# Kernel optimization log

Hardware: AMD Instinct MI355X
Metric: run time of the kernel (lower is better)

## Reference

```python
import jax, jax.numpy as jnp
import numpy as np

N_NODES = 100000
N_EDGES = 1600000
D = 128
BN_EPS = 1e-5

def setup_inputs() -> dict:
    key = jax.random.key(0)
    ks = jax.random.split(key, 6)
    h = jax.random.normal(ks[0], (N_NODES, D), dtype=jnp.float32)
    src = jax.random.randint(ks[1], (N_EDGES,), 0, N_NODES, dtype=jnp.int32)
    dst = jax.random.randint(ks[2], (N_EDGES,), 0, N_NODES, dtype=jnp.int32)
    eps = jnp.zeros((1,), dtype=jnp.float32)
    # 2-layer GIN apply_func MLP, scaled for stable activations
    W1 = jax.random.normal(ks[3], (D, D), dtype=jnp.float32) / np.sqrt(D)
    b1 = jnp.zeros((D,), dtype=jnp.float32)
    W2 = jax.random.normal(ks[4], (D, D), dtype=jnp.float32) / np.sqrt(D)
    b2 = jnp.zeros((D,), dtype=jnp.float32)
    gamma = jnp.ones((D,), dtype=jnp.float32)
    beta = jnp.zeros((D,), dtype=jnp.float32)
    return {"h": h, "src": src, "dst": dst, "eps": eps,
            "W1": W1, "b1": b1, "W2": W2, "b2": b2,
            "gamma": gamma, "beta": beta}

def reference(h, src, dst, eps, W1, b1, W2, b2, gamma, beta):
    # --- neighbor sum aggregation: update_all(copy_u('h'), fn.sum) ---
    msgs = h[src]                                   # [E, D] irregular gather
    neigh = jax.ops.segment_sum(msgs, dst, num_segments=N_NODES)  # [N, D]
    # --- eps-scaled self term ---
    x = (1.0 + eps[0]) * h + neigh                  # [N, D]
    # --- apply_func: 2-layer MLP ---
    x = jax.nn.relu(x @ W1 + b1)
    x = x @ W2 + b2
    # --- BatchNorm1d over node dim (training-mode batch stats) ---
    mean = jnp.mean(x, axis=0)
    var = jnp.mean(jnp.square(x - mean), axis=0)
    x = (x - mean) * jax.lax.rsqrt(var + BN_EPS) * gamma + beta
    # --- activation + residual ---
    x = jax.nn.relu(x)
    x = h + x  # residual (in_dim == out_dim)
    return x
```

## Files before the change

kernel.cpp:

```cpp
#include <hip/hip_runtime.h>

#define NN 100000
#define NE 1600000
#define DD 128
#define BN_EPS 1e-5f

#define SBSH 9
#define SBSZ 512
#define NSB ((NN + SBSZ - 1) / SBSZ)
#define CAPS 9216
#define SCATBLKS 512
#define EPB ((NE + SCATBLKS - 1) / SCATBLKS)
#define PREPBLKS 512
#define GRID_PS (SCATBLKS + PREPBLKS)
#define BN_BLOCKS 1024

typedef __attribute__((ext_vector_type(8))) short short8;
typedef __attribute__((ext_vector_type(4))) float floatx4;

__device__ __forceinline__ unsigned short f2bf(float f) {
    union { float f; unsigned u; } v; v.f = f;
    return (unsigned short)((v.u + 0x7FFFu + ((v.u >> 16) & 1u)) >> 16);
}
__device__ __forceinline__ float bf2f(unsigned short u) {
    union { unsigned u; float f; } v; v.u = ((unsigned)u) << 16;
    return v.f;
}

__global__ __launch_bounds__(256) void prep_scatter_kernel(
    const float* __restrict__ W1, const float* __restrict__ W2,
    unsigned short* __restrict__ W1t, unsigned short* __restrict__ W2t,
    const float* __restrict__ h, unsigned short* __restrict__ hb, int do_hb,
    const int* __restrict__ src, const int* __restrict__ dst,
    int* __restrict__ scnt, int* __restrict__ sbuf)
{
    __shared__ int bins[256];
    int t = threadIdx.x;

    if (blockIdx.x < SCATBLKS) {
        bins[t] = 0;
        __syncthreads();
        int base = blockIdx.x * EPB;
        int ecnt = min(EPB, NE - base);
        for (int i = t; i < ecnt; i += 256)
            atomicAdd(&bins[dst[base + i] >> SBSH], 1);
        __syncthreads();
        int c = bins[t];
        int gb = (t < NSB && c) ? atomicAdd(&scnt[t], c) : 0;
        __syncthreads();
        bins[t] = t * CAPS + gb;
        __syncthreads();
        for (int i = t; i < ecnt; i += 256) {
            int d = dst[base + i];
            int p = atomicAdd(&bins[d >> SBSH], 1);
            sbuf[p] = (src[base + i] << SBSH) | (d & (SBSZ - 1));
        }
    } else {
        int tid0 = (blockIdx.x - SCATBLKS) * 256 + t;
        int stride = PREPBLKS * 256;
        for (int i = tid0; i < DD * DD; i += stride) {
            int n = i >> 7, k = i & 127;
            W1t[i] = f2bf(W1[k * DD + n]);
            W2t[i] = f2bf(W2[k * DD + n]);
        }
        if (do_hb) {
            const float4* h4 = (const float4*)h;
            ushort4* hb4 = (ushort4*)hb;
            for (int i = tid0; i < NN * (DD / 4); i += stride) {
                float4 v = h4[i];
                ushort4 o;
                o.x = f2bf(v.x); o.y = f2bf(v.y); o.z = f2bf(v.z); o.w = f2bf(v.w);
                hb4[i] = o;
            }
        }
    }
}

__global__ __launch_bounds__(1024) void permute_kernel(
    const int* __restrict__ scnt, int* __restrict__ sbuf,
    int2* __restrict__ off2)
{
    __shared__ int ew[CAPS];
    __shared__ int cnt[SBSZ];
    __shared__ int cur[SBSZ];
    __shared__ int stmp[SBSZ];
    int sb = blockIdx.x, t = threadIdx.x;
    if (t < SBSZ) cnt[t] = 0;
    __syncthreads();
    int n = min(scnt[sb], CAPS);
    int sbase = sb * CAPS;
    for (int i = t; i < n; i += 1024) {
        int e = sbuf[sbase + i];
        ew[i] = e;
        atomicAdd(&cnt[e & (SBSZ - 1)], 1);
    }
    __syncthreads();
    int c = 0;
    if (t < SBSZ) { c = cnt[t]; stmp[t] = c; }
    __syncthreads();
#pragma unroll
    for (int ofs = 1; ofs < SBSZ; ofs <<= 1) {
        int u = (t < SBSZ && t >= ofs) ? stmp[t - ofs] : 0;
        __syncthreads();
        if (t < SBSZ) stmp[t] += u;
        __syncthreads();
    }
    if (t < SBSZ) {
        int excl = stmp[t] - c;
        cur[t] = excl;
        off2[sb * SBSZ + t] = make_int2(sbase + excl, sbase + excl + c);
    }
    __syncthreads();
    for (int i = t; i < n; i += 1024) {
        int e = ew[i];
        int p = atomicAdd(&cur[e & (SBSZ - 1)], 1);
        sbuf[sbase + p] = e >> SBSH;
    }
}

__global__ __launch_bounds__(256) void gather_bf16_kernel(
    const float* __restrict__ h, const unsigned short* __restrict__ hb,
    const float* __restrict__ eps, const int2* __restrict__ off2,
    const int* __restrict__ srcs, unsigned short* __restrict__ xb)
{
    int node = blockIdx.x * 16 + (threadIdx.x >> 4);
    if (node >= NN) return;
    int c8 = threadIdx.x & 15;
    const float s = 1.0f + eps[0];
    const float4* h4 = (const float4*)h;
    float4 a0 = h4[node * 32 + c8 * 2];
    float4 a1 = h4[node * 32 + c8 * 2 + 1];
    float acc[8] = {s * a0.x, s * a0.y, s * a0.z, s * a0.w,
                    s * a1.x, s * a1.y, s * a1.z, s * a1.w};
    int2 oo = off2[node];
    int e = oo.x, eend = oo.y;
    const short8* hb8 = (const short8*)hb;
    for (; e + 3 < eend; e += 4) {
        int s0 = srcs[e],     s1 = srcs[e + 1];
        int s2 = srcs[e + 2], s3 = srcs[e + 3];
        short8 v0 = hb8[s0 * 16 + c8];
        short8 v1 = hb8[s1 * 16 + c8];
        short8 v2 = hb8[s2 * 16 + c8];
        short8 v3 = hb8[s3 * 16 + c8];
#pragma unroll
        for (int j = 0; j < 8; ++j) {
            float t0 = bf2f((unsigned short)v0[j]) + bf2f((unsigned short)v1[j]);
            float t1 = bf2f((unsigned short)v2[j]) + bf2f((unsigned short)v3[j]);
            acc[j] += t0 + t1;
        }
    }
    for (; e < eend; ++e) {
        short8 v0 = hb8[srcs[e] * 16 + c8];
#pragma unroll
        for (int j = 0; j < 8; ++j) acc[j] += bf2f((unsigned short)v0[j]);
    }
    short8 o;
#pragma unroll
    for (int j = 0; j < 8; ++j) o[j] = (short)f2bf(acc[j]);
    ((short8*)xb)[node * 16 + c8] = o;
}

__global__ __launch_bounds__(256) void gather_f32_kernel(
    const float* __restrict__ h, const float* __restrict__ eps,
    const int2* __restrict__ off2, const int* __restrict__ srcs,
    unsigned short* __restrict__ xb)
{
    int node = blockIdx.x * 16 + (threadIdx.x >> 4);
    if (node >= NN) return;
    int c8 = threadIdx.x & 15;
    const float4* h4 = (const float4*)h;
    const float s = 1.0f + eps[0];
    float4 a0 = h4[node * 32 + c8 * 2];
    float4 a1 = h4[node * 32 + c8 * 2 + 1];
    float acc[8] = {s * a0.x, s * a0.y, s * a0.z, s * a0.w,
                    s * a1.x, s * a1.y, s * a1.z, s * a1.w};
    int2 oo = off2[node];
    int e = oo.x, eend = oo.y;
    for (; e + 1 < eend; e += 2) {
        int s0 = srcs[e], s1 = srcs[e + 1];
        float4 u0 = h4[s0 * 32 + c8 * 2], u1 = h4[s0 * 32 + c8 * 2 + 1];
        float4 w0 = h4[s1 * 32 + c8 * 2], w1 = h4[s1 * 32 + c8 * 2 + 1];
        acc[0] += u0.x + w0.x; acc[1] += u0.y + w0.y;
        acc[2] += u0.z + w0.z; acc[3] += u0.w + w0.w;
        acc[4] += u1.x + w1.x; acc[5] += u1.y + w1.y;
        acc[6] += u1.z + w1.z; acc[7] += u1.w + w1.w;
    }
    if (e < eend) {
        int s0 = srcs[e];
        float4 u0 = h4[s0 * 32 + c8 * 2], u1 = h4[s0 * 32 + c8 * 2 + 1];
        acc[0] += u0.x; acc[1] += u0.y; acc[2] += u0.z; acc[3] += u0.w;
        acc[4] += u1.x; acc[5] += u1.y; acc[6] += u1.z; acc[7] += u1.w;
    }
    short8 o;
#pragma unroll
    for (int j = 0; j < 8; ++j) o[j] = (short)f2bf(acc[j]);
    ((short8*)xb)[node * 16 + c8] = o;
}

__global__ __launch_bounds__(512) void mlp_fused_kernel(
    const unsigned short* __restrict__ X,
    const unsigned short* __restrict__ W1t, const unsigned short* __restrict__ W2t,
    const float* __restrict__ b1, const float* __restrict__ b2,
    unsigned short* __restrict__ Y, float* __restrict__ stats)
{
    extern __shared__ char smem[];
    unsigned short* wl = (unsigned short*)smem;
    unsigned short* xl = (unsigned short*)(smem + 34816);

    const int tid = threadIdx.x;
    const int r0 = blockIdx.x * 128;
    const int lane = tid & 63;
    const int wv = tid >> 6;
    const int m = lane & 15;
    const int hi = lane >> 4;

    const short8* W18 = (const short8*)W1t;
#pragma unroll
    for (int l = 0; l < 4; ++l) {
        int idx = tid + l * 512;
        int n = idx >> 4, c = idx & 15;
        *(short8*)&wl[n * 136 + c * 8] = W18[idx];
    }
    const short8* X8 = (const short8*)X;
#pragma unroll
    for (int l = 0; l < 4; ++l) {
        int idx = tid + l * 512;
        int row = idx >> 4, c = idx & 15;
        int g = r0 + row;
        short8 v = {0, 0, 0, 0, 0, 0, 0, 0};
        if (g < NN) v = X8[g * 16 + c];
        *(short8*)&xl[row * 136 + c * 8] = v;
    }
    __syncthreads();

    floatx4 acc[8];
#pragma unroll
    for (int i = 0; i < 8; ++i) acc[i] = (floatx4){0.f, 0.f, 0.f, 0.f};
#pragma unroll
    for (int kc = 0; kc < 4; ++kc) {
        short8 a = *(const short8*)&xl[(wv * 16 + m) * 136 + kc * 32 + hi * 8];
#pragma unroll
        for (int nt = 0; nt < 8; ++nt) {
            short8 b = *(const short8*)&wl[(nt * 16 + m) * 136 + kc * 32 + hi * 8];
            acc[nt] = __builtin_amdgcn_mfma_f32_16x16x32_bf16(a, b, acc[nt], 0, 0, 0);
        }
    }
    __syncthreads();

#pragma unroll
    for (int nt = 0; nt < 8; ++nt) {
        float bv = b1[nt * 16 + m];
#pragma unroll
        for (int r = 0; r < 4; ++r) {
            float v = fmaxf(acc[nt][r] + bv, 0.f);
            xl[(wv * 16 + hi * 4 + r) * 136 + nt * 16 + m] = f2bf(v);
        }
    }
    const short8* W28 = (const short8*)W2t;
#pragma unroll
    for (int l = 0; l < 4; ++l) {
        int idx = tid + l * 512;
        int n = idx >> 4, c = idx & 15;
        *(short8*)&wl[n * 136 + c * 8] = W28[idx];
    }
    __syncthreads();

#pragma unroll
    for (int i = 0; i < 8; ++i) acc[i] = (floatx4){0.f, 0.f, 0.f, 0.f};
#pragma unroll
    for (int kc = 0; kc < 4; ++kc) {
        short8 a = *(const short8*)&xl[(wv * 16 + m) * 136 + kc * 32 + hi * 8];
#pragma unroll
        for (int nt = 0; nt < 8; ++nt) {
            short8 b = *(const short8*)&wl[(nt * 16 + m) * 136 + kc * 32 + hi * 8];
            acc[nt] = __builtin_amdgcn_mfma_f32_16x16x32_bf16(a, b, acc[nt], 0, 0, 0);
        }
    }
    __syncthreads();

#pragma unroll
    for (int nt = 0; nt < 8; ++nt) {
        float bv = b2[nt * 16 + m];
#pragma unroll
        for (int r = 0; r < 4; ++r) {
            float v = acc[nt][r] + bv;
            xl[(wv * 16 + hi * 4 + r) * 136 + nt * 16 + m] = f2bf(v);
        }
    }
    __syncthreads();

#pragma unroll
    for (int l = 0; l < 4; ++l) {
        int idx = tid + l * 512;
        int row = idx >> 4, c = idx & 15;
        int g = r0 + row;
        if (g < NN)
            ((short8*)Y)[g * 16 + c] = *(const short8*)&xl[row * 136 + c * 8];
    }

    int col = tid & 127, quarter = tid >> 7;
    int rlim = min(128, NN - r0);
    int rbeg = quarter * 32, rend = min(rbeg + 32, rlim);
    float s = 0.f, q = 0.f;
    for (int r = rbeg; r < rend; ++r) {
        float v = bf2f(xl[r * 136 + col]);
        s += v; q += v * v;
    }
    float* red = (float*)wl;
    red[tid] = s;
    red[512 + tid] = q;
    __syncthreads();
    if (tid < 128) {
        float ts = red[tid] + red[128 + tid] + red[256 + tid] + red[384 + tid];
        float tq = red[512 + tid] + red[640 + tid] + red[768 + tid] + red[896 + tid];
        atomicAdd(&stats[tid], ts);
        atomicAdd(&stats[DD + tid], tq);
    }
}

__global__ __launch_bounds__(256) void bn_final_kernel(
    const unsigned short* __restrict__ Y, const float* __restrict__ h,
    const float* __restrict__ gamma, const float* __restrict__ beta,
    const float* __restrict__ stats, float* __restrict__ out)
{
    const float invN = 1.0f / (float)NN;
    int t0 = blockIdx.x * 256 + threadIdx.x;
    int c8 = t0 & 15;
    float sc[8], sh[8];
#pragma unroll
    for (int j = 0; j < 8; ++j) {
        int col = c8 * 8 + j;
        float mu = stats[col] * invN;
        float var = stats[DD + col] * invN - mu * mu;
        float s = rsqrtf(var + BN_EPS) * gamma[col];
        sc[j] = s;
        sh[j] = beta[col] - mu * s;
    }
    const short8* Y8 = (const short8*)Y;
    const float4* H4 = (const float4*)h;
    float4* O4 = (float4*)out;
    const int total = NN * 16;
    const int stride = BN_BLOCKS * 256;
    for (int i = t0; i < total; i += stride) {
        short8 u = Y8[i];
        float4 h0 = H4[2 * i], h1 = H4[2 * i + 1];
        float4 r0, r1;
        r0.x = h0.x + fmaxf(bf2f((unsigned short)u[0]) * sc[0] + sh[0], 0.f);
        r0.y = h0.y + fmaxf(bf2f((unsigned short)u[1]) * sc[1] + sh[1], 0.f);
        r0.z = h0.z + fmaxf(bf2f((unsigned short)u[2]) * sc[2] + sh[2], 0.f);
        r0.w = h0.w + fmaxf(bf2f((unsigned short)u[3]) * sc[3] + sh[3], 0.f);
        r1.x = h1.x + fmaxf(bf2f((unsigned short)u[4]) * sc[4] + sh[4], 0.f);
        r1.y = h1.y + fmaxf(bf2f((unsigned short)u[5]) * sc[5] + sh[5], 0.f);
        r1.z = h1.z + fmaxf(bf2f((unsigned short)u[6]) * sc[6] + sh[6], 0.f);
        r1.w = h1.w + fmaxf(bf2f((unsigned short)u[7]) * sc[7] + sh[7], 0.f);
        O4[2 * i] = r0;
        O4[2 * i + 1] = r1;
    }
}

extern "C" void kernel_launch(void* const* d_in, const int* in_sizes, int n_in,
                              void* d_out, int out_size, void* d_ws, size_t ws_size,
                              hipStream_t stream)
{
    const float* h     = (const float*)d_in[0];
    const int*   src   = (const int*)d_in[1];
    const int*   dst   = (const int*)d_in[2];
    const float* eps   = (const float*)d_in[3];
    const float* W1    = (const float*)d_in[4];
    const float* b1    = (const float*)d_in[5];
    const float* W2    = (const float*)d_in[6];
    const float* b2    = (const float*)d_in[7];
    const float* gamma = (const float*)d_in[8];
    const float* beta  = (const float*)d_in[9];
    float* out = (float*)d_out;

    char* w = (char*)d_ws;
    size_t o = 0;
    float* stats    = (float*)(w + o); o += 256 * 4;
    int* scnt       = (int*)(w + o); o += 256 * 4;
    unsigned short* W1t = (unsigned short*)(w + o); o += (size_t)DD * DD * 2;
    unsigned short* W2t = (unsigned short*)(w + o); o += (size_t)DD * DD * 2;
    int2* off2      = (int2*)(w + o); o += (size_t)NSB * SBSZ * 8;
    int* sbuf       = (int*)(w + o); o += (size_t)NSB * CAPS * 4;
    unsigned short* xb  = (unsigned short*)(w + o); o += (size_t)NN * DD * 2;
    unsigned short* hb  = (unsigned short*)(w + o); o += (size_t)NN * DD * 2;
    const int use_hb = (ws_size >= o) ? 1 : 0;

    hipMemsetAsync(stats, 0, 512 * sizeof(int), stream);

    prep_scatter_kernel<<<GRID_PS, 256, 0, stream>>>(
        W1, W2, W1t, W2t, h, hb, use_hb, src, dst, scnt, sbuf);

    permute_kernel<<<NSB, 1024, 0, stream>>>(scnt, sbuf, off2);

    if (use_hb)
        gather_bf16_kernel<<<(NN + 15) / 16, 256, 0, stream>>>(h, hb, eps, off2, sbuf, xb);
    else
        gather_f32_kernel<<<(NN + 15) / 16, 256, 0, stream>>>(h, eps, off2, sbuf, xb);

    size_t gemm_lds = 69632;
    mlp_fused_kernel<<<(NN + 127) / 128, 512, gemm_lds, stream>>>(
        xb, W1t, W2t, b1, b2, xb, stats);

    bn_final_kernel<<<BN_BLOCKS, 256, 0, stream>>>(xb, h, gamma, beta, stats, out);
}
```

Baseline: 269.3 us.

## Fuse per-superblock edge permutation into gather kernel using LDS-resident edge lists

Removes the separate permute kernel and the off2 offset buffer. Each gather block now handles a quarter (128 nodes) of a 512-node superblock: it reads that superblock's bucket of edges twice, counts and scans the edges belonging to its quarter, places the source indices into shared memory, and then runs the node-wise gather from LDS. This saves one kernel launch and the global write and reread of the permuted edges, at the cost of each bucket being read four times and a 3072-entry LDS cap that could overflow if a quarter receives more edges.

```diff
diff --git a/kernel.cpp b/kernel.cpp
--- a/kernel.cpp
+++ b/kernel.cpp
@@ -13,6 +13,7 @@
 #define EPB ((NE + SCATBLKS - 1) / SCATBLKS)
 #define PREPBLKS 512
 #define GRID_PS (SCATBLKS + PREPBLKS)
+#define QCAP 3072
 #define BN_BLOCKS 1024
 
 typedef __attribute__((ext_vector_type(8))) short short8;
@@ -76,125 +77,118 @@
     }
 }
 
-__global__ __launch_bounds__(1024) void permute_kernel(
-    const int* __restrict__ scnt, int* __restrict__ sbuf,
-    int2* __restrict__ off2)
-{
-    __shared__ int ew[CAPS];
-    __shared__ int cnt[SBSZ];
-    __shared__ int cur[SBSZ];
-    __shared__ int stmp[SBSZ];
-    int sb = blockIdx.x, t = threadIdx.x;
-    if (t < SBSZ) cnt[t] = 0;
-    __syncthreads();
-    int n = min(scnt[sb], CAPS);
-    int sbase = sb * CAPS;
-    for (int i = t; i < n; i += 1024) {
+template <bool HB>
+__global__ __launch_bounds__(256) void permgather_kernel(
+    const float* __restrict__ h, const unsigned short* __restrict__ hb,
+    const float* __restrict__ eps, const int* __restrict__ scnt,
+    const int* __restrict__ sbuf, unsigned short* __restrict__ xb)
+{
+    __shared__ int es[QCAP];
+    __shared__ int cnt[128];
+    __shared__ int beg[128];
+    __shared__ int cur[128];
+
+    const int sub = blockIdx.x;
+    const int b = sub >> 2;
+    const int q = sub & 3;
+    const int t = threadIdx.x;
+
+    if (t < 128) cnt[t] = 0;
+    __syncthreads();
+
+    const int n = min(scnt[b], CAPS);
+    const int sbase = b * CAPS;
+
+    for (int i = t; i < n; i += 256) {
         int e = sbuf[sbase + i];
-        ew[i] = e;
-        atomicAdd(&cnt[e & (SBSZ - 1)], 1);
-    }
-    __syncthreads();
-    int c = 0;
-    if (t < SBSZ) { c = cnt[t]; stmp[t] = c; }
-    __syncthreads();
-#pragma unroll
-    for (int ofs = 1; ofs < SBSZ; ofs <<= 1) {
-        int u = (t < SBSZ && t >= ofs) ? stmp[t - ofs] : 0;
-        __syncthreads();
-        if (t < SBSZ) stmp[t] += u;
-        __syncthreads();
-    }
-    if (t < SBSZ) {
-        int excl = stmp[t] - c;
-        cur[t] = excl;
-        off2[sb * SBSZ + t] = make_int2(sbase + excl, sbase + excl + c);
-    }
-    __syncthreads();
-    for (int i = t; i < n; i += 1024) {
-        int e = ew[i];
-        int p = atomicAdd(&cur[e & (SBSZ - 1)], 1);
-        sbuf[sbase + p] = e >> SBSH;
-    }
-}
-
-__global__ __launch_bounds__(256) void gather_bf16_kernel(
-    const float* __restrict__ h, const unsigned short* __restrict__ hb,
-    const float* __restrict__ eps, const int2* __restrict__ off2,
-    const int* __restrict__ srcs, unsigned short* __restrict__ xb)
-{
-    int node = blockIdx.x * 16 + (threadIdx.x >> 4);
-    if (node >= NN) return;
-    int c8 = threadIdx.x & 15;
-    const float s = 1.0f + eps[0];
+        int nl = e & (SBSZ - 1);
+        if ((nl >> 7) == q) atomicAdd(&cnt[nl & 127], 1);
+    }
+    __syncthreads();
+
+    if (t < 128) beg[t] = cnt[t];
+    __syncthreads();
+#pragma unroll
+    for (int ofs = 1; ofs < 128; ofs <<= 1) {
+        int u = (t < 128 && t >= ofs) ? beg[t - ofs] : 0;
+        __syncthreads();
+        if (t < 128) beg[t] += u;
+        __syncthreads();
+    }
+    if (t < 128) {
+        int ex = beg[t] - cnt[t];
+        beg[t] = ex;
+        cur[t] = ex;
+    }
+    __syncthreads();
+
+    for (int i = t; i < n; i += 256) {
+        int e = sbuf[sbase + i];
+        int nl = e & (SBSZ - 1);
+        if ((nl >> 7) == q) {
+            int p = atomicAdd(&cur[nl & 127], 1);
+            es[p] = e >> SBSH;
+        }
+    }
+    __syncthreads();
+
+    const float sE = 1.0f + eps[0];
     const float4* h4 = (const float4*)h;
-    float4 a0 = h4[node * 32 + c8 * 2];
-    float4 a1 = h4[node * 32 + c8 * 2 + 1];
-    float acc[8] = {s * a0.x, s * a0.y, s * a0.z, s * a0.w,
-                    s * a1.x, s * a1.y, s * a1.z, s * a1.w};
-    int2 oo = off2[node];
-    int e = oo.x, eend = oo.y;
     const short8* hb8 = (const short8*)hb;
-    for (; e + 3 < eend; e += 4) {
-        int s0 = srcs[e],     s1 = srcs[e + 1];
-        int s2 = srcs[e + 2], s3 = srcs[e + 3];
-        short8 v0 = hb8[s0 * 16 + c8];
-        short8 v1 = hb8[s1 * 16 + c8];
-        short8 v2 = hb8[s2 * 16 + c8];
-        short8 v3 = hb8[s3 * 16 + c8];
-#pragma unroll
-        for (int j = 0; j < 8; ++j) {
-            float t0 = bf2f((unsigned short)v0[j]) + bf2f((unsigned short)v1[j]);
-            float t1 = bf2f((unsigned short)v2[j]) + bf2f((unsigned short)v3[j]);
-            acc[j] += t0 + t1;
-        }
-    }
-    for (; e < eend; ++e) {
-        short8 v0 = hb8[srcs[e] * 16 + c8];
-#pragma unroll
-        for (int j = 0; j < 8; ++j) acc[j] += bf2f((unsigned short)v0[j]);
-    }
-    short8 o;
-#pragma unroll
-    for (int j = 0; j < 8; ++j) o[j] = (short)f2bf(acc[j]);
-    ((short8*)xb)[node * 16 + c8] = o;
-}
-
-__global__ __launch_bounds__(256) void gather_f32_kernel(
-    const float* __restrict__ h, const float* __restrict__ eps,
-    const int2* __restrict__ off2, const int* __restrict__ srcs,
-    unsigned short* __restrict__ xb)
-{
-    int node = blockIdx.x * 16 + (threadIdx.x >> 4);
-    if (node >= NN) return;
-    int c8 = threadIdx.x & 15;
-    const float4* h4 = (const float4*)h;
-    const float s = 1.0f + eps[0];
-    float4 a0 = h4[node * 32 + c8 * 2];
-    float4 a1 = h4[node * 32 + c8 * 2 + 1];
-    float acc[8] = {s * a0.x, s * a0.y, s * a0.z, s * a0.w,
-                    s * a1.x, s * a1.y, s * a1.z, s * a1.w};
-    int2 oo = off2[node];
-    int e = oo.x, eend = oo.y;
-    for (; e + 1 < eend; e += 2) {
-        int s0 = srcs[e], s1 = srcs[e + 1];
-        float4 u0 = h4[s0 * 32 + c8 * 2], u1 = h4[s0 * 32 + c8 * 2 + 1];
-        float4 w0 = h4[s1 * 32 + c8 * 2], w1 = h4[s1 * 32 + c8 * 2 + 1];
-        acc[0] += u0.x + w0.x; acc[1] += u0.y + w0.y;
-        acc[2] += u0.z + w0.z; acc[3] += u0.w + w0.w;
-        acc[4] += u1.x + w1.x; acc[5] += u1.y + w1.y;
-        acc[6] += u1.z + w1.z; acc[7] += u1.w + w1.w;
-    }
-    if (e < eend) {
-        int s0 = srcs[e];
-        float4 u0 = h4[s0 * 32 + c8 * 2], u1 = h4[s0 * 32 + c8 * 2 + 1];
-        acc[0] += u0.x; acc[1] += u0.y; acc[2] += u0.z; acc[3] += u0.w;
-        acc[4] += u1.x; acc[5] += u1.y; acc[6] += u1.z; acc[7] += u1.w;
-    }
-    short8 o;
-#pragma unroll
-    for (int j = 0; j < 8; ++j) o[j] = (short)f2bf(acc[j]);
-    ((short8*)xb)[node * 16 + c8] = o;
+    const int c8 = t & 15;
+    const int node0 = b * SBSZ + (q << 7);
+#pragma unroll
+    for (int pass = 0; pass < 8; ++pass) {
+        int nl = pass * 16 + (t >> 4);
+        int node = node0 + nl;
+        if (node >= NN) continue;
+        float4 a0 = h4[node * 32 + c8 * 2];
+        float4 a1 = h4[node * 32 + c8 * 2 + 1];
+        float acc[8] = {sE * a0.x, sE * a0.y, sE * a0.z, sE * a0.w,
+                        sE * a1.x, sE * a1.y, sE * a1.z, sE * a1.w};
+        int e = beg[nl], eend = beg[nl] + cnt[nl];
+        if (HB) {
+            for (; e + 3 < eend; e += 4) {
+                int s0 = es[e],     s1 = es[e + 1];
+                int s2 = es[e + 2], s3 = es[e + 3];
+                short8 v0 = hb8[s0 * 16 + c8];
+                short8 v1 = hb8[s1 * 16 + c8];
+                short8 v2 = hb8[s2 * 16 + c8];
+                short8 v3 = hb8[s3 * 16 + c8];
+#pragma unroll
+                for (int j = 0; j < 8; ++j) {
+                    float t0 = bf2f((unsigned short)v0[j]) + bf2f((unsigned short)v1[j]);
+                    float t1 = bf2f((unsigned short)v2[j]) + bf2f((unsigned short)v3[j]);
+                    acc[j] += t0 + t1;
+                }
+            }
+            for (; e < eend; ++e) {
+                short8 v0 = hb8[es[e] * 16 + c8];
+#pragma unroll
+                for (int j = 0; j < 8; ++j) acc[j] += bf2f((unsigned short)v0[j]);
+            }
+        } else {
+            for (; e + 1 < eend; e += 2) {
+                int s0 = es[e], s1 = es[e + 1];
+                float4 u0 = h4[s0 * 32 + c8 * 2], u1 = h4[s0 * 32 + c8 * 2 + 1];
+                float4 w0 = h4[s1 * 32 + c8 * 2], w1 = h4[s1 * 32 + c8 * 2 + 1];
+                acc[0] += u0.x + w0.x; acc[1] += u0.y + w0.y;
+                acc[2] += u0.z + w0.z; acc[3] += u0.w + w0.w;
+                acc[4] += u1.x + w1.x; acc[5] += u1.y + w1.y;
+                acc[6] += u1.z + w1.z; acc[7] += u1.w + w1.w;
+            }
+            if (e < eend) {
+                int s0 = es[e];
+                float4 u0 = h4[s0 * 32 + c8 * 2], u1 = h4[s0 * 32 + c8 * 2 + 1];
+                acc[0] += u0.x; acc[1] += u0.y; acc[2] += u0.z; acc[3] += u0.w;
+                acc[4] += u1.x; acc[5] += u1.y; acc[6] += u1.z; acc[7] += u1.w;
+            }
+        }
+        short8 o;
+#pragma unroll
+        for (int j = 0; j < 8; ++j) o[j] = (short)f2bf(acc[j]);
+        ((short8*)xb)[node * 16 + c8] = o;
+    }
 }
 
 __global__ __launch_bounds__(512) void mlp_fused_kernel(
@@ -380,7 +374,6 @@
     int* scnt       = (int*)(w + o); o += 256 * 4;
     unsigned short* W1t = (unsigned short*)(w + o); o += (size_t)DD * DD * 2;
     unsigned short* W2t = (unsigned short*)(w + o); o += (size_t)DD * DD * 2;
-    int2* off2      = (int2*)(w + o); o += (size_t)NSB * SBSZ * 8;
     int* sbuf       = (int*)(w + o); o += (size_t)NSB * CAPS * 4;
     unsigned short* xb  = (unsigned short*)(w + o); o += (size_t)NN * DD * 2;
     unsigned short* hb  = (unsigned short*)(w + o); o += (size_t)NN * DD * 2;
@@ -391,12 +384,10 @@
     prep_scatter_kernel<<<GRID_PS, 256, 0, stream>>>(
         W1, W2, W1t, W2t, h, hb, use_hb, src, dst, scnt, sbuf);
 
-    permute_kernel<<<NSB, 1024, 0, stream>>>(scnt, sbuf, off2);
-
     if (use_hb)
-        gather_bf16_kernel<<<(NN + 15) / 16, 256, 0, stream>>>(h, hb, eps, off2, sbuf, xb);
+        permgather_kernel<true><<<NSB * 4, 256, 0, stream>>>(h, hb, eps, scnt, sbuf, xb);
     else
-        gather_f32_kernel<<<(NN + 15) / 16, 256, 0, stream>>>(h, eps, off2, sbuf, xb);
+        permgather_kernel<false><<<NSB * 4, 256, 0, stream>>>(h, hb, eps, scnt, sbuf, xb);
 
     size_t gemm_lds = 69632;
     mlp_fused_kernel<<<(NN + 127) / 128, 512, gemm_lds, stream>>>(
```

After: 278.3 us. +3.4%, slower.
